# Kernel tuning notes

Hardware: AMD Instinct MI355X
Metric: run time of the kernel (lower is better)

The kernel has to match this reference:

```python
import jax, jax.numpy as jnp
import numpy as np

B, S, D, H = 2, 2048, 1024, 16
HD = D // H
SPARSITY = 0.5
NEG_INF = jnp.float32(-jnp.inf)


def setup_inputs() -> dict:
    key = jax.random.key(0)
    ks = jax.random.split(key, 12)
    s = 1.0 / np.sqrt(D)
    inp = {
        "query": jax.random.normal(ks[0], (B, S, D), jnp.float32),
        "key": jax.random.normal(ks[1], (B, S, D), jnp.float32),
        "value": jax.random.normal(ks[2], (B, S, D), jnp.float32),
        "Wq": jax.random.uniform(ks[3], (D, D), jnp.float32, -s, s),
        "bq": jax.random.uniform(ks[4], (D,), jnp.float32, -s, s),
        "Wk": jax.random.uniform(ks[5], (D, D), jnp.float32, -s, s),
        "bk": jax.random.uniform(ks[6], (D,), jnp.float32, -s, s),
        "Wv": jax.random.uniform(ks[7], (D, D), jnp.float32, -s, s),
        "bv": jax.random.uniform(ks[8], (D,), jnp.float32, -s, s),
        "Wo": jax.random.uniform(ks[9], (D, D), jnp.float32, -s, s),
        "bo": jax.random.uniform(ks[10], (D,), jnp.float32, -s, s),
    }
    return inp


def reference(query, key, value, Wq, bq, Wk, bk, Wv, bv, Wo, bo):
    b, sq, _ = query.shape
    sk = key.shape[1]
    # projections -> [b, h, s, hd]
    Q = (query @ Wq.T + bq).reshape(b, sq, H, HD).transpose(0, 2, 1, 3)
    K = (key @ Wk.T + bk).reshape(b, sk, H, HD).transpose(0, 2, 1, 3)
    V = (value @ Wv.T + bv).reshape(b, sk, H, HD).transpose(0, 2, 1, 3)
    scale = jnp.float32(HD ** -0.5)
    scores = jnp.einsum('bhqd,bhkd->bhqk', Q, K) * scale  # [b,h,sq,sk]
    # top-k sparsification: keep k largest scores per query row, rest -> -inf
    k = max(1, int(sk * (1.0 - SPARSITY)))
    topk_vals, _ = jax.lax.top_k(scores, k)
    thresh = topk_vals[..., -1:]  # k-th largest value per row
    scores = jnp.where(scores >= thresh, scores, NEG_INF)
    attn = jax.nn.softmax(scores, axis=-1)  # dropout p=0.0 -> identity
    out = jnp.einsum('bhqk,bhkd->bhqd', attn, V)
    out = out.transpose(0, 2, 1, 3).reshape(b, sq, D)
    out = out @ Wo.T + bo
    return out, attn
```

## Files before the change

kernel.cpp:

```cpp
#include <hip/hip_runtime.h>
#include <math.h>

#define Bb 2
#define Ss 2048
#define Dd 1024
#define Hh 16
#define HDd 64
#define KSEL 1024
#define MROWS 4096

__device__ __forceinline__ unsigned f2u(float f) {
    unsigned u = __float_as_uint(f);
    return (u & 0x80000000u) ? ~u : (u | 0x80000000u);
}

template <int TRANSPOSED>
__device__ __forceinline__ void gemm_body_1024(const float* __restrict__ X,
                                               const float* __restrict__ W,
                                               const float* __restrict__ bias,
                                               float* __restrict__ Y,
                                               int m0, int n0) {
    const int tid = threadIdx.x;
    const int tx = tid & 15, ty = tid >> 4;

    __shared__ __align__(16) float As[16][128];
    __shared__ __align__(16) float Bs[16][128];

    float acc[8][8];
#pragma unroll
    for (int i = 0; i < 8; ++i)
#pragma unroll
        for (int j = 0; j < 8; ++j) acc[i][j] = 0.f;

    for (int k0 = 0; k0 < 1024; k0 += 16) {
#pragma unroll
        for (int c = 0; c < 2; ++c) {
            int idx = tid + c * 256;
            int row = idx >> 2;
            int kq  = (idx & 3) << 2;
            float4 va = *(const float4*)&X[(size_t)(m0 + row) * 1024 + k0 + kq];
            As[kq + 0][row] = va.x; As[kq + 1][row] = va.y;
            As[kq + 2][row] = va.z; As[kq + 3][row] = va.w;
            float4 vb = *(const float4*)&W[(size_t)(n0 + row) * 1024 + k0 + kq];
            Bs[kq + 0][row] = vb.x; Bs[kq + 1][row] = vb.y;
            Bs[kq + 2][row] = vb.z; Bs[kq + 3][row] = vb.w;
        }
        __syncthreads();
#pragma unroll
        for (int kk = 0; kk < 16; ++kk) {
            float a[8], b[8];
            *(float4*)&a[0] = *(const float4*)&As[kk][ty * 4];
            *(float4*)&a[4] = *(const float4*)&As[kk][64 + ty * 4];
            *(float4*)&b[0] = *(const float4*)&Bs[kk][tx * 4];
            *(float4*)&b[4] = *(const float4*)&Bs[kk][64 + tx * 4];
#pragma unroll
            for (int i = 0; i < 8; ++i)
#pragma unroll
                for (int j = 0; j < 8; ++j) acc[i][j] = fmaf(a[i], b[j], acc[i][j]);
        }
        __syncthreads();
    }

#pragma unroll
    for (int i = 0; i < 8; ++i) {
        int m = m0 + ((i < 4) ? (ty * 4 + i) : (64 + ty * 4 + i - 4));
#pragma unroll
        for (int jq = 0; jq < 2; ++jq) {
            int n = n0 + jq * 64 + tx * 4;
            float4 bv = *(const float4*)&bias[n];
            float4 v;
            v.x = acc[i][jq * 4 + 0] + bv.x;
            v.y = acc[i][jq * 4 + 1] + bv.y;
            v.z = acc[i][jq * 4 + 2] + bv.z;
            v.w = acc[i][jq * 4 + 3] + bv.w;
            if (TRANSPOSED) {
                int bi = m >> 11, s = m & 2047;
                int h = n >> 6, d = n & 63;
                *(float4*)&Y[(((size_t)(bi * Hh + h)) * Ss + s) * HDd + d] = v;
            } else {
                *(float4*)&Y[(size_t)m * 1024 + n] = v;
            }
        }
    }
}

__global__ __launch_bounds__(256) void qkv_kernel(
    const float* __restrict__ q, const float* __restrict__ k, const float* __restrict__ v,
    const float* __restrict__ Wq, const float* __restrict__ Wk, const float* __restrict__ Wv,
    const float* __restrict__ bq, const float* __restrict__ bk, const float* __restrict__ bv,
    float* __restrict__ Qo, float* __restrict__ Ko, float* __restrict__ Vo) {
    int z = blockIdx.z;
    const float* X = (z == 0) ? q : ((z == 1) ? k : v);
    const float* W = (z == 0) ? Wq : ((z == 1) ? Wk : Wv);
    const float* bias = (z == 0) ? bq : ((z == 1) ? bk : bv);
    float* Y = (z == 0) ? Qo : ((z == 1) ? Ko : Vo);
    gemm_body_1024<1>(X, W, bias, Y, blockIdx.y * 128, blockIdx.x * 128);
}

__global__ __launch_bounds__(256) void outproj_kernel(
    const float* __restrict__ O, const float* __restrict__ Wo,
    const float* __restrict__ bo, float* __restrict__ Y) {
    gemm_body_1024<0>(O, Wo, bo, Y, blockIdx.y * 128, blockIdx.x * 128);
}

__global__ __launch_bounds__(256) void scores_kernel(const float* __restrict__ Q,
                                                     const float* __restrict__ Kd,
                                                     float* __restrict__ Sc) {
    const int tid = threadIdx.x;
    const int tx = tid & 15, ty = tid >> 4;
    const int z = blockIdx.z;
    const int m0 = blockIdx.y * 128;
    const int n0 = blockIdx.x * 128;
    const float* Qz = Q + (size_t)z * Ss * HDd;
    const float* Kz = Kd + (size_t)z * Ss * HDd;
    float* Cz = Sc + (size_t)z * Ss * Ss;

    __shared__ __align__(16) float As[16][128];
    __shared__ __align__(16) float Bs[16][128];

    float acc[8][8];
#pragma unroll
    for (int i = 0; i < 8; ++i)
#pragma unroll
        for (int j = 0; j < 8; ++j) acc[i][j] = 0.f;

    for (int k0 = 0; k0 < 64; k0 += 16) {
#pragma unroll
        for (int c = 0; c < 2; ++c) {
            int idx = tid + c * 256;
            int row = idx >> 2;
            int kq  = (idx & 3) << 2;
            float4 va = *(const float4*)&Qz[(size_t)(m0 + row) * 64 + k0 + kq];
            As[kq + 0][row] = va.x; As[kq + 1][row] = va.y;
            As[kq + 2][row] = va.z; As[kq + 3][row] = va.w;
            float4 vb = *(const float4*)&Kz[(size_t)(n0 + row) * 64 + k0 + kq];
            Bs[kq + 0][row] = vb.x; Bs[kq + 1][row] = vb.y;
            Bs[kq + 2][row] = vb.z; Bs[kq + 3][row] = vb.w;
        }
        __syncthreads();
#pragma unroll
        for (int kk = 0; kk < 16; ++kk) {
            float a[8], b[8];
            *(float4*)&a[0] = *(const float4*)&As[kk][ty * 4];
            *(float4*)&a[4] = *(const float4*)&As[kk][64 + ty * 4];
            *(float4*)&b[0] = *(const float4*)&Bs[kk][tx * 4];
            *(float4*)&b[4] = *(const float4*)&Bs[kk][64 + tx * 4];
#pragma unroll
            for (int i = 0; i < 8; ++i)
#pragma unroll
                for (int j = 0; j < 8; ++j) acc[i][j] = fmaf(a[i], b[j], acc[i][j]);
        }
        __syncthreads();
    }

#pragma unroll
    for (int i = 0; i < 8; ++i) {
        int m = m0 + ((i < 4) ? (ty * 4 + i) : (64 + ty * 4 + i - 4));
#pragma unroll
        for (int jq = 0; jq < 2; ++jq) {
            int n = n0 + jq * 64 + tx * 4;
            float4 v;
            v.x = acc[i][jq * 4 + 0] * 0.125f;
            v.y = acc[i][jq * 4 + 1] * 0.125f;
            v.z = acc[i][jq * 4 + 2] * 0.125f;
            v.w = acc[i][jq * 4 + 3] * 0.125f;
            *(float4*)&Cz[(size_t)m * Ss + n] = v;
        }
    }
}

__global__ __launch_bounds__(256) void topk_softmax_kernel(float* __restrict__ Sc) {
    const int tid = threadIdx.x;
    const int hrow = ((tid >> 6) << 1) | (tid & 1);
    float* p = Sc + (size_t)blockIdx.x * Ss;

    __shared__ unsigned hist[8][260];
    __shared__ unsigned shist[256];
    __shared__ unsigned gs[16];
    __shared__ float red[256];
    __shared__ unsigned sel[2];
    __shared__ float fred[2];

    float f[8];
    unsigned ubits[8];
#pragma unroll
    for (int j = 0; j < 8; ++j) {
        f[j] = p[tid + j * 256];
        ubits[j] = f2u(f[j]);
    }

    unsigned prefix = 0, rk = KSEL;
    for (int pass = 0; pass < 4; ++pass) {
        const int shift = 24 - pass * 8;
        for (int i = tid; i < 8 * 260; i += 256) (&hist[0][0])[i] = 0u;
        __syncthreads();
#pragma unroll
        for (int j = 0; j < 8; ++j) {
            unsigned u = ubits[j];
            bool ok = (pass == 0) ? true : ((u >> (shift + 8)) == prefix);
            if (ok) atomicAdd(&hist[hrow][(u >> shift) & 255u], 1u);
        }
        __syncthreads();
        unsigned bc = 0;
#pragma unroll
        for (int r = 0; r < 8; ++r) bc += hist[r][tid];
        shist[tid] = bc;
        __syncthreads();
        if (tid < 16) {
            unsigned s = 0;
            for (int i = 0; i < 16; ++i) s += shist[tid * 16 + i];
            gs[tid] = s;
        }
        __syncthreads();
        if (tid == 0) {
            unsigned run = 0;
            int g = 15;
            for (; g > 0; --g) {
                unsigned c = gs[g];
                if (run + c >= rk) break;
                run += c;
            }
            unsigned need = rk - run;
            unsigned run2 = 0;
            int b = g * 16 + 15;
            for (; b > g * 16; --b) {
                unsigned c = shist[b];
                if (run2 + c >= need) break;
                run2 += c;
            }
            sel[0] = (unsigned)b;
            sel[1] = need - run2;
        }
        __syncthreads();
        prefix = (prefix << 8) | sel[0];
        rk = sel[1];
    }
    const unsigned uth = prefix;

    float lm = -INFINITY;
#pragma unroll
    for (int j = 0; j < 8; ++j) lm = fmaxf(lm, f[j]);
    red[tid] = lm;
    __syncthreads();
    if (tid < 32) {
        float m = red[tid];
#pragma unroll
        for (int i = 1; i < 8; ++i) m = fmaxf(m, red[tid + 32 * i]);
        red[tid] = m;
    }
    __syncthreads();
    if (tid == 0) {
        float m = red[0];
        for (int i = 1; i < 32; ++i) m = fmaxf(m, red[i]);
        fred[0] = m;
    }
    __syncthreads();
    const float mx = fred[0];

    float e[8];
    float ls = 0.f;
#pragma unroll
    for (int j = 0; j < 8; ++j) {
        float ev = (ubits[j] >= uth) ? __expf(f[j] - mx) : 0.f;
        e[j] = ev;
        ls += ev;
    }
    red[tid] = ls;
    __syncthreads();
    if (tid < 32) {
        float s2 = red[tid];
#pragma unroll
        for (int i = 1; i < 8; ++i) s2 += red[tid + 32 * i];
        red[tid] = s2;
    }
    __syncthreads();
    if (tid == 0) {
        float s2 = red[0];
        for (int i = 1; i < 32; ++i) s2 += red[i];
        fred[1] = s2;
    }
    __syncthreads();
    const float inv = 1.f / fred[1];

#pragma unroll
    for (int j = 0; j < 8; ++j) p[tid + j * 256] = e[j] * inv;
}

__global__ __launch_bounds__(256) void pv_kernel(const float* __restrict__ A,
                                                 const float* __restrict__ V,
                                                 float* __restrict__ O) {
    const int tid = threadIdx.x;
    const int tx = tid & 15, ty = tid >> 4;
    const int z = blockIdx.y;
    const int m0 = blockIdx.x * 128;
    const int bi = z >> 4, h = z & 15;
    const float* Az = A + (size_t)z * Ss * Ss;
    const float* Vz = V + (size_t)z * Ss * HDd;

    __shared__ __align__(16) float As[32][128];
    __shared__ __align__(16) float Bs[32][64];

    float acc[8][4];
#pragma unroll
    for (int i = 0; i < 8; ++i)
#pragma unroll
        for (int j = 0; j < 4; ++j) acc[i][j] = 0.f;

    for (int k0 = 0; k0 < Ss; k0 += 32) {
#pragma unroll
        for (int c = 0; c < 4; ++c) {
            int idx = tid + c * 256;
            int row = idx >> 3;
            int kq  = (idx & 7) << 2;
            float4 va = *(const float4*)&Az[(size_t)(m0 + row) * Ss + k0 + kq];
            As[kq + 0][row] = va.x; As[kq + 1][row] = va.y;
            As[kq + 2][row] = va.z; As[kq + 3][row] = va.w;
        }
#pragma unroll
        for (int c = 0; c < 2; ++c) {
            int idx = tid + c * 256;
            int kr = idx >> 4;
            int dq = (idx & 15) << 2;
            *(float4*)&Bs[kr][dq] = *(const float4*)&Vz[(size_t)(k0 + kr) * 64 + dq];
        }
        __syncthreads();
#pragma unroll
        for (int kk = 0; kk < 32; ++kk) {
            float a[8], b[4];
            *(float4*)&a[0] = *(const float4*)&As[kk][ty * 8];
            *(float4*)&a[4] = *(const float4*)&As[kk][ty * 8 + 4];
            *(float4*)&b[0] = *(const float4*)&Bs[kk][tx * 4];
#pragma unroll
            for (int i = 0; i < 8; ++i)
#pragma unroll
                for (int j = 0; j < 4; ++j) acc[i][j] = fmaf(a[i], b[j], acc[i][j]);
        }
        __syncthreads();
    }

#pragma unroll
    for (int i = 0; i < 8; ++i) {
        int srow = m0 + ty * 8 + i;
        float4 v = {acc[i][0], acc[i][1], acc[i][2], acc[i][3]};
        *(float4*)&O[((size_t)(bi * Ss + srow)) * Dd + h * 64 + tx * 4] = v;
    }
}

extern "C" void kernel_launch(void* const* d_in, const int* in_sizes, int n_in,
                              void* d_out, int out_size, void* d_ws, size_t ws_size,
                              hipStream_t stream) {
    const float* q  = (const float*)d_in[0];
    const float* k  = (const float*)d_in[1];
    const float* v  = (const float*)d_in[2];
    const float* Wq = (const float*)d_in[3];
    const float* bq = (const float*)d_in[4];
    const float* Wk = (const float*)d_in[5];
    const float* bk = (const float*)d_in[6];
    const float* Wv = (const float*)d_in[7];
    const float* bv = (const float*)d_in[8];
    const float* Wo = (const float*)d_in[9];
    const float* bo = (const float*)d_in[10];

    float* out  = (float*)d_out;
    float* attn = out + (size_t)Bb * Ss * Dd;

    float* ws = (float*)d_ws;
    const size_t SZ = (size_t)Bb * Ss * Dd;
    float* Qb = ws;
    float* Kb = ws + SZ;
    float* Vb = ws + 2 * SZ;
    float* Ob = ws + 3 * SZ;

    dim3 blk(256);

    qkv_kernel<<<dim3(8, 32, 3), blk, 0, stream>>>(q, k, v, Wq, Wk, Wv, bq, bk, bv, Qb, Kb, Vb);
    scores_kernel<<<dim3(16, 16, 32), blk, 0, stream>>>(Qb, Kb, attn);
    topk_softmax_kernel<<<dim3(65536), blk, 0, stream>>>(attn);
    pv_kernel<<<dim3(16, 32), blk, 0, stream>>>(attn, Vb, Ob);
    outproj_kernel<<<dim3(8, 32), blk, 0, stream>>>(Ob, Wo, bo, out);
}
```

Measured before the change: 1.707 ms.

## Use 3-pass 12/10/10-bit radix select and vectorized row IO in top-k softmax

Replaces the four-pass 8-bit radix select with three passes (12, 10 and 10 bits) over a single shared histogram, using a three-level hierarchical scan to locate the threshold bucket. This removes one histogram pass and its barriers per row, at the cost of more atomic contention on the non-replicated histogram. Row loads and stores now use float4 with a contiguous per-thread layout instead of strided scalar accesses.

```diff
diff --git a/kernel.cpp b/kernel.cpp
--- a/kernel.cpp
+++ b/kernel.cpp
@@ -171,69 +171,134 @@
 
 __global__ __launch_bounds__(256) void topk_softmax_kernel(float* __restrict__ Sc) {
     const int tid = threadIdx.x;
-    const int hrow = ((tid >> 6) << 1) | (tid & 1);
     float* p = Sc + (size_t)blockIdx.x * Ss;
 
-    __shared__ unsigned hist[8][260];
-    __shared__ unsigned shist[256];
-    __shared__ unsigned gs[16];
+    __shared__ __align__(16) unsigned hist[4096];
+    __shared__ unsigned gs[256];
+    __shared__ unsigned ggs[16];
     __shared__ float red[256];
     __shared__ unsigned sel[2];
     __shared__ float fred[2];
 
     float f[8];
     unsigned ubits[8];
-#pragma unroll
-    for (int j = 0; j < 8; ++j) {
-        f[j] = p[tid + j * 256];
-        ubits[j] = f2u(f[j]);
-    }
-
-    unsigned prefix = 0, rk = KSEL;
-    for (int pass = 0; pass < 4; ++pass) {
-        const int shift = 24 - pass * 8;
-        for (int i = tid; i < 8 * 260; i += 256) (&hist[0][0])[i] = 0u;
-        __syncthreads();
-#pragma unroll
-        for (int j = 0; j < 8; ++j) {
-            unsigned u = ubits[j];
-            bool ok = (pass == 0) ? true : ((u >> (shift + 8)) == prefix);
-            if (ok) atomicAdd(&hist[hrow][(u >> shift) & 255u], 1u);
-        }
-        __syncthreads();
-        unsigned bc = 0;
-#pragma unroll
-        for (int r = 0; r < 8; ++r) bc += hist[r][tid];
-        shist[tid] = bc;
+    {
+        float4 a = *(const float4*)&p[tid * 4];
+        float4 b = *(const float4*)&p[1024 + tid * 4];
+        f[0] = a.x; f[1] = a.y; f[2] = a.z; f[3] = a.w;
+        f[4] = b.x; f[5] = b.y; f[6] = b.z; f[7] = b.w;
+    }
+#pragma unroll
+    for (int j = 0; j < 8; ++j) ubits[j] = f2u(f[j]);
+
+    unsigned rk = KSEL;
+    unsigned prefix = 0;
+
+    uint4 zz; zz.x = 0u; zz.y = 0u; zz.z = 0u; zz.w = 0u;
+
+    {
+#pragma unroll
+        for (int q = 0; q < 4; ++q) *(uint4*)&hist[tid * 16 + q * 4] = zz;
+        __syncthreads();
+#pragma unroll
+        for (int j = 0; j < 8; ++j) atomicAdd(&hist[ubits[j] >> 20], 1u);
+        __syncthreads();
+        unsigned s = 0;
+#pragma unroll
+        for (int q = 0; q < 4; ++q) {
+            uint4 hv = *(const uint4*)&hist[tid * 16 + q * 4];
+            s += hv.x + hv.y + hv.z + hv.w;
+        }
+        gs[tid] = s;
         __syncthreads();
         if (tid < 16) {
-            unsigned s = 0;
-            for (int i = 0; i < 16; ++i) s += shist[tid * 16 + i];
-            gs[tid] = s;
+            unsigned t2 = 0;
+            for (int i = 0; i < 16; ++i) t2 += gs[tid * 16 + i];
+            ggs[tid] = t2;
         }
         __syncthreads();
         if (tid == 0) {
             unsigned run = 0;
             int g = 15;
-            for (; g > 0; --g) {
-                unsigned c = gs[g];
-                if (run + c >= rk) break;
-                run += c;
-            }
-            unsigned need = rk - run;
-            unsigned run2 = 0;
-            int b = g * 16 + 15;
-            for (; b > g * 16; --b) {
-                unsigned c = shist[b];
-                if (run2 + c >= need) break;
-                run2 += c;
-            }
+            for (; g > 0; --g) { unsigned c = ggs[g]; if (run + c >= rk) break; run += c; }
+            int sg = g * 16 + 15;
+            for (; sg > g * 16; --sg) { unsigned c = gs[sg]; if (run + c >= rk) break; run += c; }
+            int b = sg * 16 + 15;
+            for (; b > sg * 16; --b) { unsigned c = hist[b]; if (run + c >= rk) break; run += c; }
+            sel[0] = (unsigned)b; sel[1] = rk - run;
+        }
+        __syncthreads();
+        prefix = sel[0];
+        rk = sel[1];
+    }
+
+    {
+        *(uint4*)&hist[tid * 4] = zz;
+        __syncthreads();
+#pragma unroll
+        for (int j = 0; j < 8; ++j) {
+            if ((ubits[j] >> 20) == prefix)
+                atomicAdd(&hist[(ubits[j] >> 10) & 1023u], 1u);
+        }
+        __syncthreads();
+        {
+            uint4 hv = *(const uint4*)&hist[tid * 4];
+            gs[tid] = hv.x + hv.y + hv.z + hv.w;
+        }
+        __syncthreads();
+        if (tid < 16) {
+            unsigned t2 = 0;
+            for (int i = 0; i < 16; ++i) t2 += gs[tid * 16 + i];
+            ggs[tid] = t2;
+        }
+        __syncthreads();
+        if (tid == 0) {
+            unsigned run = 0;
+            int g = 15;
+            for (; g > 0; --g) { unsigned c = ggs[g]; if (run + c >= rk) break; run += c; }
+            int sg = g * 16 + 15;
+            for (; sg > g * 16; --sg) { unsigned c = gs[sg]; if (run + c >= rk) break; run += c; }
+            int b = sg * 4 + 3;
+            for (; b > sg * 4; --b) { unsigned c = hist[b]; if (run + c >= rk) break; run += c; }
+            sel[0] = (unsigned)b; sel[1] = rk - run;
+        }
+        __syncthreads();
+        prefix = (prefix << 10) | sel[0];
+        rk = sel[1];
+    }
+
+    {
+        *(uint4*)&hist[tid * 4] = zz;
+        __syncthreads();
+#pragma unroll
+        for (int j = 0; j < 8; ++j) {
+            if ((ubits[j] >> 10) == prefix)
+                atomicAdd(&hist[ubits[j] & 1023u], 1u);
+        }
+        __syncthreads();
+        {
+            uint4 hv = *(const uint4*)&hist[tid * 4];
+            gs[tid] = hv.x + hv.y + hv.z + hv.w;
+        }
+        __syncthreads();
+        if (tid < 16) {
+            unsigned t2 = 0;
+            for (int i = 0; i < 16; ++i) t2 += gs[tid * 16 + i];
+            ggs[tid] = t2;
+        }
+        __syncthreads();
+        if (tid == 0) {
+            unsigned run = 0;
+            int g = 15;
+            for (; g > 0; --g) { unsigned c = ggs[g]; if (run + c >= rk) break; run += c; }
+            int sg = g * 16 + 15;
+            for (; sg > g * 16; --sg) { unsigned c = gs[sg]; if (run + c >= rk) break; run += c; }
+            int b = sg * 4 + 3;
+            for (; b > sg * 4; --b) { unsigned c = hist[b]; if (run + c >= rk) break; run += c; }
             sel[0] = (unsigned)b;
-            sel[1] = need - run2;
-        }
-        __syncthreads();
-        prefix = (prefix << 8) | sel[0];
-        rk = sel[1];
+        }
+        __syncthreads();
+        prefix = (prefix << 10) | sel[0];
     }
     const unsigned uth = prefix;
 
@@ -282,8 +347,13 @@
     __syncthreads();
     const float inv = 1.f / fred[1];
 
-#pragma unroll
-    for (int j = 0; j < 8; ++j) p[tid + j * 256] = e[j] * inv;
+    {
+        float4 o;
+        o.x = e[0] * inv; o.y = e[1] * inv; o.z = e[2] * inv; o.w = e[3] * inv;
+        *(float4*)&p[tid * 4] = o;
+        o.x = e[4] * inv; o.y = e[5] * inv; o.z = e[6] * inv; o.w = e[7] * inv;
+        *(float4*)&p[1024 + tid * 4] = o;
+    }
 }
 
 __global__ __launch_bounds__(256) void pv_kernel(const float* __restrict__ A,
```

Result: faster. 1.672 ms (-2.1%).
